# Performance work log

Measured on AMD Instinct MI355X. Metric: run time of the kernel, lower is better.

Reference implementation:

```python
import jax, jax.numpy as jnp
import numpy as np

N_PREV = 8191
DIMS = 4096


def setup_inputs() -> dict:
    key = jax.random.key(0)
    k1, k2, k3, k4, k5 = jax.random.split(key, 5)
    prev_inps = jax.random.normal(k1, (N_PREV, DIMS), dtype=jnp.float32)
    inp = jax.random.normal(k2, (DIMS,), dtype=jnp.float32)
    # learned parameters, init std=0.01 as in the torch module
    W_Q = jax.random.normal(k3, (DIMS, DIMS), dtype=jnp.float32) * 0.01
    W_K = jax.random.normal(k4, (DIMS, DIMS), dtype=jnp.float32) * 0.01
    W_V = jax.random.normal(k5, (DIMS, DIMS), dtype=jnp.float32) * 0.01
    return {"prev_inps": prev_inps, "inp": inp, "W_Q": W_Q, "W_K": W_K, "W_V": W_V}


def reference(prev_inps, inp, W_Q, W_K, W_V):
    # One masked self-attention decode step.
    inputs = jnp.concatenate([prev_inps, inp[None, :]], axis=0)  # (n+1, d)
    query = W_Q @ inp                                            # (d,)
    keys = jnp.einsum('md,nd->nm', W_K, inputs)                  # (n+1, d)
    values = jnp.einsum('md,nd->nm', W_V, inputs)                # (n+1, d)
    logits = keys @ query                                        # (n+1,)
    aweights = jax.nn.softmax(logits, axis=-1)                   # (n+1,)
    context = aweights @ values                                  # (d,)
    output = context + inp                                       # residual
    return (output, inputs)
```

## Files before the change

kernel.cpp:

```cpp
#include <hip/hip_runtime.h>
#include <math.h>

#define D      4096
#define NPREV  8191
#define NROWS  8192
#define FB     512
#define FR     16

typedef float f4 __attribute__((ext_vector_type(4)));

static __device__ __forceinline__ f4 nt_load4(const float* p) {
    return __builtin_nontemporal_load(reinterpret_cast<const f4*>(p));
}
static __device__ __forceinline__ f4 ld4(const float* p) {
    return *reinterpret_cast<const f4*>(p);
}
static __device__ __forceinline__ void st4(f4 v, float* p) {
    *reinterpret_cast<f4*>(p) = v;
}

template<bool RESIDUAL>
__global__ void k_matvec_rows(const float* __restrict__ W, const float* __restrict__ v,
                              const float* __restrict__ resid, float* __restrict__ out) {
    int row  = blockIdx.x * 4 + (threadIdx.x >> 6);
    int lane = threadIdx.x & 63;
    const float* Wrow = W + (size_t)row * D;
    float acc = 0.f;
    #pragma unroll
    for (int i = 0; i < 16; ++i) {
        int c = lane + i * 64;
        f4 w = nt_load4(Wrow + 4 * c);
        f4 x = ld4(v + 4 * c);
        acc += w.x * x.x + w.y * x.y + w.z * x.z + w.w * x.w;
    }
    #pragma unroll
    for (int off = 32; off; off >>= 1) acc += __shfl_down(acc, off, 64);
    if (lane == 0) out[row] = RESIDUAL ? (acc + resid[row]) : acc;
}

__global__ void k_kq(const float* __restrict__ W, const float* __restrict__ q,
                     float* __restrict__ kq) {
    __shared__ float s_q[D];
    __shared__ f4 s_part[64][4];
    int t = threadIdx.x;
    int b = blockIdx.x;
    for (int i = t; i < D; i += 256) s_q[i] = q[i];
    __syncthreads();
    int c4 = b * 4 + (t & 3);
    int r0 = t >> 2;
    f4 acc = (f4)0.f;
    #pragma unroll 16
    for (int i = 0; i < 64; ++i) {
        int m = r0 + i * 64;
        acc += s_q[m] * nt_load4(W + (size_t)m * D + 4 * c4);
    }
    s_part[r0][t & 3] = acc;
    __syncthreads();
    if (t < 4) {
        f4 a = (f4)0.f;
        #pragma unroll
        for (int g = 0; g < 64; ++g) a += s_part[g][t];
        st4(a, kq + 4 * (b * 4 + t));
    }
}

__global__ __launch_bounds__(1024) void k_flash_copy(
        const float* __restrict__ prev, const float* __restrict__ inp,
        const float* __restrict__ kq, float* __restrict__ io,
        float* __restrict__ ms, float* __restrict__ ctxpart) {
    const int b    = blockIdx.x;
    const int slot = b & 7;
    const int grp  = b >> 3;
    const int role = grp & 1;
    const int wk   = (grp >> 1) * 8 + slot;
    const int n0   = wk * FR;
    const int t    = threadIdx.x;

    if (role == 1) {
        #pragma unroll 4
        for (int r = 0; r < FR; ++r) {
            int n = n0 + r;
            const float* src = (n < NPREV) ? (prev + (size_t)n * D) : inp;
            st4(ld4(src + 4 * t), io + (size_t)n * D + 4 * t);
        }
        return;
    }

    __shared__ float s_wred[16][FR];
    __shared__ float s_log[FR];
    const int wid = t >> 6, lane = t & 63;
    const f4 kqv = ld4(kq + 4 * t);

    float p[FR];
    #pragma unroll
    for (int r = 0; r < FR; ++r) {
        int n = n0 + r;
        const float* src = (n < NPREV) ? (prev + (size_t)n * D) : inp;
        f4 x = ld4(src + 4 * t);
        p[r] = x.x * kqv.x + x.y * kqv.y + x.z * kqv.z + x.w * kqv.w;
    }
    #pragma unroll
    for (int r = 0; r < FR; ++r) {
        float v = p[r];
        #pragma unroll
        for (int off = 32; off; off >>= 1) v += __shfl_down(v, off, 64);
        if (lane == 0) s_wred[wid][r] = v;
    }
    __syncthreads();
    if (t < FR) {
        float s = 0.f;
        #pragma unroll
        for (int w = 0; w < 16; ++w) s += s_wred[w][t];
        s_log[t] = s;
    }
    __syncthreads();
    float m_b = -INFINITY;
    #pragma unroll
    for (int r = 0; r < FR; ++r) m_b = fmaxf(m_b, s_log[r]);
    float e[FR], s_b = 0.f;
    #pragma unroll
    for (int r = 0; r < FR; ++r) { e[r] = __expf(s_log[r] - m_b); s_b += e[r]; }
    f4 a = (f4)0.f;
    #pragma unroll
    for (int r = 0; r < FR; ++r) {
        int n = n0 + r;
        const float* src = (n < NPREV) ? (prev + (size_t)n * D) : inp;
        a += e[r] * ld4(src + 4 * t);
    }
    st4(a, ctxpart + (size_t)wk * D + 4 * t);
    if (t == 0) { ms[2 * wk] = m_b; ms[2 * wk + 1] = s_b; }
}

template<int FBT>
__global__ void k_combine(const float* __restrict__ ms, const float* __restrict__ ctxpart,
                          float* __restrict__ ctx) {
    constexpr int PPT = FBT / 256;
    constexpr int PPG = FBT / 16;
    __shared__ float s_w[FBT];
    __shared__ float s_red[8];
    __shared__ f4 s_acc[16][16];
    int t = threadIdx.x;
    int lane = t & 63, wid = t >> 6;
    float mloc[PPT];
    float mx = -INFINITY;
    #pragma unroll
    for (int k = 0; k < PPT; ++k) { mloc[k] = ms[2 * (t + 256 * k)]; mx = fmaxf(mx, mloc[k]); }
    #pragma unroll
    for (int off = 32; off; off >>= 1) mx = fmaxf(mx, __shfl_down(mx, off, 64));
    if (lane == 0) s_red[wid] = mx;
    __syncthreads();
    float M = fmaxf(fmaxf(s_red[0], s_red[1]), fmaxf(s_red[2], s_red[3]));
    float sc = 0.f;
    #pragma unroll
    for (int k = 0; k < PPT; ++k) {
        float w = __expf(mloc[k] - M);
        s_w[t + 256 * k] = w;
        sc += w * ms[2 * (t + 256 * k) + 1];
    }
    #pragma unroll
    for (int off = 32; off; off >>= 1) sc += __shfl_down(sc, off, 64);
    if (lane == 0) s_red[4 + wid] = sc;
    __syncthreads();
    float S = s_red[4] + s_red[5] + s_red[6] + s_red[7];
    int c = t & 15, g = t >> 4;
    int col4 = blockIdx.x * 16 + c;
    f4 a = (f4)0.f;
    #pragma unroll 8
    for (int i = 0; i < PPG; ++i) {
        int pp = g * PPG + i;
        a += s_w[pp] * ld4(ctxpart + (size_t)pp * D + 4 * col4);
    }
    s_acc[g][c] = a;
    __syncthreads();
    if (t < 16) {
        f4 aa = (f4)0.f;
        #pragma unroll
        for (int gg = 0; gg < 16; ++gg) aa += s_acc[gg][t];
        st4(aa * (1.f / S), ctx + 4 * (blockIdx.x * 16 + t));
    }
}

extern "C" void kernel_launch(void* const* d_in, const int* in_sizes, int n_in,
                              void* d_out, int out_size, void* d_ws, size_t ws_size,
                              hipStream_t stream) {
    const float* prev = (const float*)d_in[0];
    const float* inp  = (const float*)d_in[1];
    const float* W_Q  = (const float*)d_in[2];
    const float* W_K  = (const float*)d_in[3];
    const float* W_V  = (const float*)d_in[4];
    float* out = (float*)d_out;
    float* io  = out + D;
    float* ws  = (float*)d_ws;

    float* q       = ws;
    float* kq      = q + D;
    float* ms      = kq + D;
    float* ctxpart = ms + 2 * FB;
    float* ctx     = ctxpart + (size_t)FB * D;

    k_matvec_rows<false><<<1024, 256, 0, stream>>>(W_Q, inp, nullptr, q);
    k_kq<<<256, 256, 0, stream>>>(W_K, q, kq);
    k_flash_copy<<<1024, 1024, 0, stream>>>(prev, inp, kq, io, ms, ctxpart);
    k_combine<FB><<<64, 256, 0, stream>>>(ms, ctxpart, ctx);
    k_matvec_rows<true><<<1024, 256, 0, stream>>>(W_V, ctx, inp, out);
}
```

Measured before the change: 126.8 us.

## Fuse input copy into flash attention pass with one wave per row logits

Merges the separate copy-role blocks into the flash kernel so each wave reads a row of the inputs, writes it to the output copy and computes its logit in the same pass. Each wave now owns one row and reduces it with a single shuffle tree, which removes the cross-wave shared-memory reduction. The grid halves to FB blocks with a launch-bounds occupancy hint. The second pass over the rows for the weighted sum is kept and is expected to hit in cache. Risks are lower parallelism and register pressure from the occupancy hint.

```diff
diff --git a/kernel.cpp b/kernel.cpp
--- a/kernel.cpp
+++ b/kernel.cpp
@@ -5,7 +5,7 @@
 #define NPREV  8191
 #define NROWS  8192
 #define FB     512
-#define FR     16
+#define FR     (NROWS / FB)
 
 typedef float f4 __attribute__((ext_vector_type(4)));
 
@@ -64,71 +64,53 @@
     }
 }
 
-__global__ __launch_bounds__(1024) void k_flash_copy(
+__global__ __launch_bounds__(1024, 8) void k_flash(
         const float* __restrict__ prev, const float* __restrict__ inp,
         const float* __restrict__ kq, float* __restrict__ io,
         float* __restrict__ ms, float* __restrict__ ctxpart) {
-    const int b    = blockIdx.x;
-    const int slot = b & 7;
-    const int grp  = b >> 3;
-    const int role = grp & 1;
-    const int wk   = (grp >> 1) * 8 + slot;
-    const int n0   = wk * FR;
-    const int t    = threadIdx.x;
+    __shared__ float s_log[FR];
+    __shared__ float s_e[FR];
+    const int n0 = blockIdx.x * FR;
+    const int t = threadIdx.x;
+    const int wid = t >> 6, lane = t & 63;
 
-    if (role == 1) {
+    {
+        const int r = wid;
+        const int n = n0 + r;
+        const float* src = (n < NPREV) ? (prev + (size_t)n * D) : inp;
+        float* dst = io + (size_t)n * D;
+        float acc = 0.f;
         #pragma unroll 4
-        for (int r = 0; r < FR; ++r) {
-            int n = n0 + r;
-            const float* src = (n < NPREV) ? (prev + (size_t)n * D) : inp;
-            st4(ld4(src + 4 * t), io + (size_t)n * D + 4 * t);
+        for (int i = lane; i < D / 4; i += 64) {
+            f4 x = ld4(src + 4 * i);
+            f4 k = ld4(kq + 4 * i);
+            st4(x, dst + 4 * i);
+            acc += x.x * k.x + x.y * k.y + x.z * k.z + x.w * k.w;
         }
-        return;
+        #pragma unroll
+        for (int off = 32; off; off >>= 1) acc += __shfl_down(acc, off, 64);
+        if (lane == 0) s_log[r] = acc;
     }
+    __syncthreads();
 
-    __shared__ float s_wred[16][FR];
-    __shared__ float s_log[FR];
-    const int wid = t >> 6, lane = t & 63;
-    const f4 kqv = ld4(kq + 4 * t);
+    float m_b = -INFINITY;
+    #pragma unroll
+    for (int r = 0; r < FR; ++r) m_b = fmaxf(m_b, s_log[r]);
+    if (t < FR) s_e[t] = __expf(s_log[t] - m_b);
+    __syncthreads();
+    float s_b = 0.f;
+    #pragma unroll
+    for (int r = 0; r < FR; ++r) s_b += s_e[r];
 
-    float p[FR];
-    #pragma unroll
+    f4 a = (f4)0.f;
+    #pragma unroll 4
     for (int r = 0; r < FR; ++r) {
         int n = n0 + r;
         const float* src = (n < NPREV) ? (prev + (size_t)n * D) : inp;
-        f4 x = ld4(src + 4 * t);
-        p[r] = x.x * kqv.x + x.y * kqv.y + x.z * kqv.z + x.w * kqv.w;
+        a += s_e[r] * ld4(src + 4 * t);
     }
-    #pragma unroll
-    for (int r = 0; r < FR; ++r) {
-        float v = p[r];
-        #pragma unroll
-        for (int off = 32; off; off >>= 1) v += __shfl_down(v, off, 64);
-        if (lane == 0) s_wred[wid][r] = v;
-    }
-    __syncthreads();
-    if (t < FR) {
-        float s = 0.f;
-        #pragma unroll
-        for (int w = 0; w < 16; ++w) s += s_wred[w][t];
-        s_log[t] = s;
-    }
-    __syncthreads();
-    float m_b = -INFINITY;
-    #pragma unroll
-    for (int r = 0; r < FR; ++r) m_b = fmaxf(m_b, s_log[r]);
-    float e[FR], s_b = 0.f;
-    #pragma unroll
-    for (int r = 0; r < FR; ++r) { e[r] = __expf(s_log[r] - m_b); s_b += e[r]; }
-    f4 a = (f4)0.f;
-    #pragma unroll
-    for (int r = 0; r < FR; ++r) {
-        int n = n0 + r;
-        const float* src = (n < NPREV) ? (prev + (size_t)n * D) : inp;
-        a += e[r] * ld4(src + 4 * t);
-    }
-    st4(a, ctxpart + (size_t)wk * D + 4 * t);
-    if (t == 0) { ms[2 * wk] = m_b; ms[2 * wk + 1] = s_b; }
+    st4(a, ctxpart + (size_t)blockIdx.x * D + 4 * t);
+    if (t == 0) { ms[2 * blockIdx.x] = m_b; ms[2 * blockIdx.x + 1] = s_b; }
 }
 
 template<int FBT>
@@ -200,7 +182,7 @@
 
     k_matvec_rows<false><<<1024, 256, 0, stream>>>(W_Q, inp, nullptr, q);
     k_kq<<<256, 256, 0, stream>>>(W_K, q, kq);
-    k_flash_copy<<<1024, 1024, 0, stream>>>(prev, inp, kq, io, ms, ctxpart);
+    k_flash<<<FB, 1024, 0, stream>>>(prev, inp, kq, io, ms, ctxpart);
     k_combine<FB><<<64, 256, 0, stream>>>(ms, ctxpart, ctx);
     k_matvec_rows<true><<<1024, 256, 0, stream>>>(W_V, ctx, inp, out);
 }
```

Measured after the change: 124.4 us. No clear change (-1.9%).
